# Kernel tuning notes

Hardware: AMD Instinct MI355X
Metric: run time of the kernel (lower is better)

## Reference

```python
import jax, jax.numpy as jnp
import numpy as np

NI = 50000      # input nodes
NO = 50000      # output nodes
DEG = 16        # uniform neighborhood size -> E = NO*DEG
E = NO * DEG
FI = 64         # input feature dim
UNITS = 64
D = 3           # coord feature dim


def setup_inputs() -> dict:
    key = jax.random.key(0)
    k1, k2, k3, k4 = jax.random.split(key, 4)
    node_features = jax.random.normal(k1, (NI, FI), dtype=jnp.float32)
    coord_features = jax.random.normal(k2, (E, D), dtype=jnp.float32)
    indices = jax.random.randint(k3, (E,), 0, NI, dtype=jnp.int64)
    # uniform ragged structure: each output node has DEG edges
    row_splits = (jnp.arange(NO + 1, dtype=jnp.int64) * DEG)
    W = jax.random.normal(k4, (FI, UNITS * D), dtype=jnp.float32) * (1.0 / np.sqrt(FI))
    b = jnp.zeros((UNITS * D,), dtype=jnp.float32)
    return {"node_features": node_features, "coord_features": coord_features,
            "indices": indices, "row_splits": row_splits, "W": W, "b": b}


def reference(node_features, coord_features, indices, row_splits, W, b):
    # Dense projection on input nodes: [Ni, units*D]
    h = node_features @ W + b
    # gather_first=False path of ragged_convolution_transpose: gather after dense
    g = h[indices]                       # [E, units*D]
    g = g.reshape(-1, UNITS, D)          # [E, units, D]
    # contract over coord dim: f_eu = sum_d g_eud * coord_ed
    f = jnp.einsum('eud,ed->eu', g, coord_features)  # [E, units]
    # activation is None (identity)
    # ragged segment-sum via row_splits -> segment ids per edge
    num_out = row_splits.shape[0] - 1
    row_lengths = jnp.diff(row_splits)
    seg_ids = jnp.repeat(jnp.arange(num_out), row_lengths,
                         total_repeat_length=f.shape[0])
    out = jax.ops.segment_sum(f, seg_ids, num_segments=num_out)  # [No, units]
    return out
```

## Files before the change

kernel.cpp:

```cpp
#include <hip/hip_runtime.h>


#define NO 50000
#define NI 50000
#define DEG 16
#define FI 64
#define UNITS 64
#define KK 192
#define TN 16
#define NSTEP 6
#define GPAD 200
#define NBLK 1024
#define NTILES (NO / TN)
#define NFELEM (NI * FI)

typedef __attribute__((ext_vector_type(8))) short short8;
typedef __attribute__((ext_vector_type(4))) float float4v;
typedef __attribute__((ext_vector_type(4))) unsigned short ushort4v;

static __device__ __forceinline__ unsigned int asu(float x){ union{float f;unsigned int u;}c; c.f=x; return c.u; }
static __device__ __forceinline__ float asf(unsigned int x){ union{unsigned int u;float f;}c; c.u=x; return c.f; }
static __device__ __forceinline__ float rdlane_f(float v, int l){
    return asf((unsigned int)__builtin_amdgcn_readlane((int)asu(v), l));
}
static __device__ __forceinline__ unsigned short f2bf_rne(float x){
    const unsigned int v = asu(x);
    return (unsigned short)((v + 0x7FFFu + ((v >> 16) & 1u)) >> 16);
}

__global__ __launch_bounds__(256)
void rct3_cvt(const float* __restrict__ nf, unsigned short* __restrict__ nf16)
{
    const int i = blockIdx.x * 256 + threadIdx.x;
    const float4v v = ((const float4v*)nf)[i];
    ushort4v o;
    o[0] = f2bf_rne(v[0]); o[1] = f2bf_rne(v[1]);
    o[2] = f2bf_rne(v[2]); o[3] = f2bf_rne(v[3]);
    ((ushort4v*)nf16)[i] = o;
}

template<bool BF16>
__global__ __launch_bounds__(256, 4)
void rct3(const float* __restrict__ nf, const unsigned short* __restrict__ nf16,
          const float* __restrict__ coord, const int* __restrict__ idx,
          const float* __restrict__ W, const float* __restrict__ b,
          float* __restrict__ out)
{
    __shared__ __align__(16) unsigned short Ghi[2][TN][GPAD];
    __shared__ __align__(16) float Cs[2][TN][4];

    const int tid  = threadIdx.x;
    const int w    = tid >> 6;
    const int lane = tid & 63;
    const int m16  = lane & 15;
    const int quad = lane >> 4;

    const int u = 16 * w + m16;
    short8 Bf[NSTEP];
    #pragma unroll
    for (int s = 0; s < NSTEP; ++s) {
        #pragma unroll
        for (int j = 0; j < 8; ++j) {
            const int k = s * 32 + quad * 8 + j;
            const int i = k / 3, d = k - 3 * i;
            Bf[s][j] = (short)f2bf_rne(W[i * KK + 3 * u + d]);
        }
    }
    const float b0 = b[3*u+0], b1 = b[3*u+1], b2 = b[3*u+2];

    int t = blockIdx.x;
    int   vid;
    float cv0, cv1, cv2;
    {
        const int e = (t * TN + 4 * w) * DEG + lane;
        vid = __builtin_nontemporal_load(&idx[e]);
        cv0 = __builtin_nontemporal_load(&coord[3*e+0]);
        cv1 = __builtin_nontemporal_load(&coord[3*e+1]);
        cv2 = __builtin_nontemporal_load(&coord[3*e+2]);
    }

    int pp = 0;
    for (; t < NTILES; t += NBLK, pp ^= 1) {
        const int node0 = t * TN;

        const int t2 = t + NBLK;
        int   vidN = 0;
        float cv0N = 0.f, cv1N = 0.f, cv2N = 0.f;
        if (t2 < NTILES) {
            const int e2 = (t2 * TN + 4 * w) * DEG + lane;
            vidN = __builtin_nontemporal_load(&idx[e2]);
            cv0N = __builtin_nontemporal_load(&coord[3*e2+0]);
            cv1N = __builtin_nontemporal_load(&coord[3*e2+1]);
            cv2N = __builtin_nontemporal_load(&coord[3*e2+2]);
        }

        {
            float s0 = cv0, s1 = cv1, s2 = cv2;
            #pragma unroll
            for (int m = 1; m <= 8; m <<= 1) {
                s0 += __shfl_xor(s0, m, 64);
                s1 += __shfl_xor(s1, m, 64);
                s2 += __shfl_xor(s2, m, 64);
            }
            if ((lane & 15) == 0) {
                float4v cc = {s0, s1, s2, 0.f};
                *(float4v*)(&Cs[pp][4*w + (lane >> 4)][0]) = cc;
            }
        }

        #pragma unroll
        for (int r = 0; r < 4; ++r) {
            const int n = 4 * w + r;
            float a0 = 0.f, a1 = 0.f, a2 = 0.f;
            #pragma unroll
            for (int j = 0; j < DEG; ++j) {
                const int l  = 16 * r + j;
                const int id = __builtin_amdgcn_readlane(vid, l);
                const float c0 = rdlane_f(cv0, l);
                const float c1 = rdlane_f(cv1, l);
                const float c2 = rdlane_f(cv2, l);
                float v;
                if constexpr (BF16) {
                    v = asf(((unsigned int)nf16[id * FI + lane]) << 16);
                } else {
                    v = nf[id * FI + lane];
                }
                a0 += v * c0; a1 += v * c1; a2 += v * c2;
            }
            Ghi[pp][n][3*lane+0] = f2bf_rne(a0);
            Ghi[pp][n][3*lane+1] = f2bf_rne(a1);
            Ghi[pp][n][3*lane+2] = f2bf_rne(a2);
        }
        __syncthreads();

        float4v acc = {0.f, 0.f, 0.f, 0.f};
        #pragma unroll
        for (int s = 0; s < NSTEP; ++s) {
            const short8 Ahi = *(const short8*)(&Ghi[pp][m16][s*32 + quad*8]);
            acc = __builtin_amdgcn_mfma_f32_16x16x32_bf16(Ahi, Bf[s], acc, 0, 0, 0);
        }

        #pragma unroll
        for (int reg = 0; reg < 4; ++reg) {
            const int row = quad * 4 + reg;
            const float4v c = *(const float4v*)(&Cs[pp][row][0]);
            out[(node0 + row) * UNITS + u] =
                acc[reg] + c[0]*b0 + c[1]*b1 + c[2]*b2;
        }

        vid = vidN; cv0 = cv0N; cv1 = cv1N; cv2 = cv2N;
    }
}

extern "C" void kernel_launch(void* const* d_in, const int* in_sizes, int n_in,
                              void* d_out, int out_size, void* d_ws, size_t ws_size,
                              hipStream_t stream) {
    const float* nf    = (const float*)d_in[0];
    const float* coord = (const float*)d_in[1];
    const int*   idx   = (const int*)d_in[2];
    const float* W     = (const float*)d_in[4];
    const float* b     = (const float*)d_in[5];
    float* out = (float*)d_out;

    if (ws_size >= (size_t)NFELEM * sizeof(unsigned short)) {
        unsigned short* nf16 = (unsigned short*)d_ws;
        rct3_cvt<<<dim3(NFELEM / 4 / 256), dim3(256), 0, stream>>>(nf, nf16);
        rct3<true><<<dim3(NBLK), dim3(256), 0, stream>>>(
            nf, nf16, coord, idx, W, b, out);
    } else {
        rct3<false><<<dim3(NBLK), dim3(256), 0, stream>>>(
            nf, nullptr, coord, idx, W, b, out);
    }
}
```

Measured before the change: 108.0 us.

## Replace persistent tile loop with one block per tile and raise occupancy

The persistent grid of 1024 blocks, which looped over tiles with double-buffered shared memory and prefetched the next tile's indices and coords, becomes one block per 16-node tile (3125 blocks) with single-buffered shared memory. Each block now issues its idx/coord loads before building the bf16 W fragments, so the two overlap. The launch-bounds occupancy hint rises from 4 to 6 blocks per CU. Each block now rebuilds the W fragments from global memory, which the persistent loop did only once per block, and loses the cross-tile prefetch. In exchange it gains more resident waves to hide gather latency and removes the loop's tail imbalance.

```diff
diff --git a/kernel.cpp b/kernel.cpp
--- a/kernel.cpp
+++ b/kernel.cpp
@@ -10,7 +10,6 @@
 #define TN 16
 #define NSTEP 6
 #define GPAD 200
-#define NBLK 1024
 #define NTILES (NO / TN)
 #define NFELEM (NI * FI)
 
@@ -40,20 +39,33 @@
 }
 
 template<bool BF16>
-__global__ __launch_bounds__(256, 4)
+__global__ __launch_bounds__(256, 6)
 void rct3(const float* __restrict__ nf, const unsigned short* __restrict__ nf16,
           const float* __restrict__ coord, const int* __restrict__ idx,
           const float* __restrict__ W, const float* __restrict__ b,
           float* __restrict__ out)
 {
-    __shared__ __align__(16) unsigned short Ghi[2][TN][GPAD];
-    __shared__ __align__(16) float Cs[2][TN][4];
+    __shared__ __align__(16) unsigned short Ghi[TN][GPAD];
+    __shared__ __align__(16) float Cs[TN][4];
 
     const int tid  = threadIdx.x;
     const int w    = tid >> 6;
     const int lane = tid & 63;
     const int m16  = lane & 15;
     const int quad = lane >> 4;
+
+    const int t     = blockIdx.x;
+    const int node0 = t * TN;
+
+    int   vid;
+    float cv0, cv1, cv2;
+    {
+        const int e = (node0 + 4 * w) * DEG + lane;
+        vid = __builtin_nontemporal_load(&idx[e]);
+        cv0 = __builtin_nontemporal_load(&coord[3*e+0]);
+        cv1 = __builtin_nontemporal_load(&coord[3*e+1]);
+        cv2 = __builtin_nontemporal_load(&coord[3*e+2]);
+    }
 
     const int u = 16 * w + m16;
     short8 Bf[NSTEP];
@@ -68,87 +80,58 @@
     }
     const float b0 = b[3*u+0], b1 = b[3*u+1], b2 = b[3*u+2];
 
-    int t = blockIdx.x;
-    int   vid;
-    float cv0, cv1, cv2;
     {
-        const int e = (t * TN + 4 * w) * DEG + lane;
-        vid = __builtin_nontemporal_load(&idx[e]);
-        cv0 = __builtin_nontemporal_load(&coord[3*e+0]);
-        cv1 = __builtin_nontemporal_load(&coord[3*e+1]);
-        cv2 = __builtin_nontemporal_load(&coord[3*e+2]);
+        float s0 = cv0, s1 = cv1, s2 = cv2;
+        #pragma unroll
+        for (int m = 1; m <= 8; m <<= 1) {
+            s0 += __shfl_xor(s0, m, 64);
+            s1 += __shfl_xor(s1, m, 64);
+            s2 += __shfl_xor(s2, m, 64);
+        }
+        if ((lane & 15) == 0) {
+            float4v cc = {s0, s1, s2, 0.f};
+            *(float4v*)(&Cs[4*w + (lane >> 4)][0]) = cc;
+        }
     }
 
-    int pp = 0;
-    for (; t < NTILES; t += NBLK, pp ^= 1) {
-        const int node0 = t * TN;
+    #pragma unroll
+    for (int r = 0; r < 4; ++r) {
+        const int n = 4 * w + r;
+        float a0 = 0.f, a1 = 0.f, a2 = 0.f;
+        #pragma unroll
+        for (int j = 0; j < DEG; ++j) {
+            const int l  = 16 * r + j;
+            const int id = __builtin_amdgcn_readlane(vid, l);
+            const float c0 = rdlane_f(cv0, l);
+            const float c1 = rdlane_f(cv1, l);
+            const float c2 = rdlane_f(cv2, l);
+            float v;
+            if constexpr (BF16) {
+                v = asf(((unsigned int)nf16[id * FI + lane]) << 16);
+            } else {
+                v = nf[id * FI + lane];
+            }
+            a0 += v * c0; a1 += v * c1; a2 += v * c2;
+        }
+        Ghi[n][3*lane+0] = f2bf_rne(a0);
+        Ghi[n][3*lane+1] = f2bf_rne(a1);
+        Ghi[n][3*lane+2] = f2bf_rne(a2);
+    }
+    __syncthreads();
 
-        const int t2 = t + NBLK;
-        int   vidN = 0;
-        float cv0N = 0.f, cv1N = 0.f, cv2N = 0.f;
-        if (t2 < NTILES) {
-            const int e2 = (t2 * TN + 4 * w) * DEG + lane;
-            vidN = __builtin_nontemporal_load(&idx[e2]);
-            cv0N = __builtin_nontemporal_load(&coord[3*e2+0]);
-            cv1N = __builtin_nontemporal_load(&coord[3*e2+1]);
-            cv2N = __builtin_nontemporal_load(&coord[3*e2+2]);
-        }
+    float4v acc = {0.f, 0.f, 0.f, 0.f};
+    #pragma unroll
+    for (int s = 0; s < NSTEP; ++s) {
+        const short8 Ahi = *(const short8*)(&Ghi[m16][s*32 + quad*8]);
+        acc = __builtin_amdgcn_mfma_f32_16x16x32_bf16(Ahi, Bf[s], acc, 0, 0, 0);
+    }
 
-        {
-            float s0 = cv0, s1 = cv1, s2 = cv2;
-            #pragma unroll
-            for (int m = 1; m <= 8; m <<= 1) {
-                s0 += __shfl_xor(s0, m, 64);
-                s1 += __shfl_xor(s1, m, 64);
-                s2 += __shfl_xor(s2, m, 64);
-            }
-            if ((lane & 15) == 0) {
-                float4v cc = {s0, s1, s2, 0.f};
-                *(float4v*)(&Cs[pp][4*w + (lane >> 4)][0]) = cc;
-            }
-        }
-
-        #pragma unroll
-        for (int r = 0; r < 4; ++r) {
-            const int n = 4 * w + r;
-            float a0 = 0.f, a1 = 0.f, a2 = 0.f;
-            #pragma unroll
-            for (int j = 0; j < DEG; ++j) {
-                const int l  = 16 * r + j;
-                const int id = __builtin_amdgcn_readlane(vid, l);
-                const float c0 = rdlane_f(cv0, l);
-                const float c1 = rdlane_f(cv1, l);
-                const float c2 = rdlane_f(cv2, l);
-                float v;
-                if constexpr (BF16) {
-                    v = asf(((unsigned int)nf16[id * FI + lane]) << 16);
-                } else {
-                    v = nf[id * FI + lane];
-                }
-                a0 += v * c0; a1 += v * c1; a2 += v * c2;
-            }
-            Ghi[pp][n][3*lane+0] = f2bf_rne(a0);
-            Ghi[pp][n][3*lane+1] = f2bf_rne(a1);
-            Ghi[pp][n][3*lane+2] = f2bf_rne(a2);
-        }
-        __syncthreads();
-
-        float4v acc = {0.f, 0.f, 0.f, 0.f};
-        #pragma unroll
-        for (int s = 0; s < NSTEP; ++s) {
-            const short8 Ahi = *(const short8*)(&Ghi[pp][m16][s*32 + quad*8]);
-            acc = __builtin_amdgcn_mfma_f32_16x16x32_bf16(Ahi, Bf[s], acc, 0, 0, 0);
-        }
-
-        #pragma unroll
-        for (int reg = 0; reg < 4; ++reg) {
-            const int row = quad * 4 + reg;
-            const float4v c = *(const float4v*)(&Cs[pp][row][0]);
-            out[(node0 + row) * UNITS + u] =
-                acc[reg] + c[0]*b0 + c[1]*b1 + c[2]*b2;
-        }
-
-        vid = vidN; cv0 = cv0N; cv1 = cv1N; cv2 = cv2N;
+    #pragma unroll
+    for (int reg = 0; reg < 4; ++reg) {
+        const int row = quad * 4 + reg;
+        const float4v c = *(const float4v*)(&Cs[row][0]);
+        out[(node0 + row) * UNITS + u] =
+            acc[reg] + c[0]*b0 + c[1]*b1 + c[2]*b2;
     }
 }
 
@@ -165,10 +148,10 @@
     if (ws_size >= (size_t)NFELEM * sizeof(unsigned short)) {
         unsigned short* nf16 = (unsigned short*)d_ws;
         rct3_cvt<<<dim3(NFELEM / 4 / 256), dim3(256), 0, stream>>>(nf, nf16);
-        rct3<true><<<dim3(NBLK), dim3(256), 0, stream>>>(
+        rct3<true><<<dim3(NTILES), dim3(256), 0, stream>>>(
             nf, nf16, coord, idx, W, b, out);
     } else {
-        rct3<false><<<dim3(NBLK), dim3(256), 0, stream>>>(
+        rct3<false><<<dim3(NTILES), dim3(256), 0, stream>>>(
             nf, nullptr, coord, idx, W, b, out);
     }
 }
```

Result: slower. 116.4 us (+7.8%).

## Stage gathered bf16 neighbor rows into LDS with 16-byte vector loads

Applied to the files above, without the earlier changes.

Replaces the per-edge 2-byte scalar gathers of bf16 node features with a cooperative pass. Each wave loads its 64 neighbor rows as 16-byte vectors into registers, writes them to a per-wave LDS buffer, and the contraction loop then reads from LDS. The goal is fewer, wider global memory transactions on the gather. The shared-memory double buffer is dropped in favour of an extra barrier per tile, and LDS use rises to about 32KB per block, which may reduce occupancy.

```diff
diff --git a/kernel.cpp b/kernel.cpp
--- a/kernel.cpp
+++ b/kernel.cpp
@@ -16,6 +16,7 @@
 
 typedef __attribute__((ext_vector_type(8))) short short8;
 typedef __attribute__((ext_vector_type(4))) float float4v;
+typedef __attribute__((ext_vector_type(4))) unsigned int uint4v;
 typedef __attribute__((ext_vector_type(4))) unsigned short ushort4v;
 
 static __device__ __forceinline__ unsigned int asu(float x){ union{float f;unsigned int u;}c; c.f=x; return c.u; }
@@ -46,8 +47,9 @@
           const float* __restrict__ W, const float* __restrict__ b,
           float* __restrict__ out)
 {
-    __shared__ __align__(16) unsigned short Ghi[2][TN][GPAD];
-    __shared__ __align__(16) float Cs[2][TN][4];
+    __shared__ __align__(16) unsigned short Snf[4][64][64];
+    __shared__ __align__(16) unsigned short Ghi[TN][GPAD];
+    __shared__ __align__(16) float Cs[TN][4];
 
     const int tid  = threadIdx.x;
     const int w    = tid >> 6;
@@ -79,8 +81,7 @@
         cv2 = __builtin_nontemporal_load(&coord[3*e+2]);
     }
 
-    int pp = 0;
-    for (; t < NTILES; t += NBLK, pp ^= 1) {
+    for (; t < NTILES; t += NBLK) {
         const int node0 = t * TN;
 
         const int t2 = t + NBLK;
@@ -94,6 +95,8 @@
             cv2N = __builtin_nontemporal_load(&coord[3*e2+2]);
         }
 
+        __syncthreads();
+
         {
             float s0 = cv0, s1 = cv1, s2 = cv2;
             #pragma unroll
@@ -104,7 +107,22 @@
             }
             if ((lane & 15) == 0) {
                 float4v cc = {s0, s1, s2, 0.f};
-                *(float4v*)(&Cs[pp][4*w + (lane >> 4)][0]) = cc;
+                *(float4v*)(&Cs[4*w + (lane >> 4)][0]) = cc;
+            }
+        }
+
+        if constexpr (BF16) {
+            uint4v rowreg[8];
+            #pragma unroll
+            for (int i = 0; i < 8; ++i) {
+                const int src = 8 * i + (lane >> 3);
+                const int id  = __shfl(vid, src, 64);
+                rowreg[i] = *(const uint4v*)((const char*)nf16 +
+                              (unsigned long long)id * (FI * 2) + (lane & 7) * 16);
+            }
+            #pragma unroll
+            for (int i = 0; i < 8; ++i) {
+                *(uint4v*)((char*)&Snf[w][0][0] + i * 1024 + lane * 16) = rowreg[i];
             }
         }
 
@@ -115,35 +133,35 @@
             #pragma unroll
             for (int j = 0; j < DEG; ++j) {
                 const int l  = 16 * r + j;
-                const int id = __builtin_amdgcn_readlane(vid, l);
                 const float c0 = rdlane_f(cv0, l);
                 const float c1 = rdlane_f(cv1, l);
                 const float c2 = rdlane_f(cv2, l);
                 float v;
                 if constexpr (BF16) {
-                    v = asf(((unsigned int)nf16[id * FI + lane]) << 16);
+                    v = asf(((unsigned int)Snf[w][l][lane]) << 16);
                 } else {
+                    const int id = __builtin_amdgcn_readlane(vid, l);
                     v = nf[id * FI + lane];
                 }
                 a0 += v * c0; a1 += v * c1; a2 += v * c2;
             }
-            Ghi[pp][n][3*lane+0] = f2bf_rne(a0);
-            Ghi[pp][n][3*lane+1] = f2bf_rne(a1);
-            Ghi[pp][n][3*lane+2] = f2bf_rne(a2);
+            Ghi[n][3*lane+0] = f2bf_rne(a0);
+            Ghi[n][3*lane+1] = f2bf_rne(a1);
+            Ghi[n][3*lane+2] = f2bf_rne(a2);
         }
         __syncthreads();
 
         float4v acc = {0.f, 0.f, 0.f, 0.f};
         #pragma unroll
         for (int s = 0; s < NSTEP; ++s) {
-            const short8 Ahi = *(const short8*)(&Ghi[pp][m16][s*32 + quad*8]);
+            const short8 Ahi = *(const short8*)(&Ghi[m16][s*32 + quad*8]);
             acc = __builtin_amdgcn_mfma_f32_16x16x32_bf16(Ahi, Bf[s], acc, 0, 0, 0);
         }
 
         #pragma unroll
         for (int reg = 0; reg < 4; ++reg) {
             const int row = quad * 4 + reg;
-            const float4v c = *(const float4v*)(&Cs[pp][row][0]);
+            const float4v c = *(const float4v*)(&Cs[row][0]);
             out[(node0 + row) * UNITS + u] =
                 acc[reg] + c[0]*b0 + c[1]*b1 + c[2]*b2;
         }
```

New measurement: 107.9 us. Within noise of the previous version (-0.1%).
